# Kernel optimization log

Hardware: AMD Instinct MI355X
Metric: run time of the kernel (lower is better)

Reference implementation:

```python
import jax, jax.numpy as jnp
import numpy as np

H_DIM_EXP = 25  # n = 2**25 = 33,554,432

def setup_inputs() -> dict:
    key = jax.random.key(0)
    x = jax.random.normal(key, (2 ** H_DIM_EXP,), dtype=jnp.float32)
    return {"x": x, "h_dim_exp": H_DIM_EXP}

def reference(x, h_dim_exp):
    # Fast Walsh-Hadamard transform. The original views x as [1,2,2,...,2,1]
    # and applies a (+,-) butterfly along each of the log2(n) axes-of-size-2.
    # Butterfly stages on distinct bits commute, so we process bits from low
    # to high with rank-3 reshapes instead of a rank-(exp+2) tensor.
    y = x
    for i in range(h_dim_exp):
        y = y.reshape(-1, 2, 2 ** i)        # (n/2^{i+1}, 2, 2^i)
        a, b = y[:, 0, :], y[:, 1, :]
        y = jnp.stack([a + b, a - b], axis=1)
    return y.reshape(x.shape)
```

## Files before the change

### kernel.cpp

```cpp
#include <hip/hip_runtime.h>


typedef float vf4 __attribute__((ext_vector_type(4)));

__device__ __forceinline__ float4 ntload(const float4* p) {
  vf4 r = __builtin_nontemporal_load(reinterpret_cast<const vf4*>(p));
  return *reinterpret_cast<float4*>(&r);
}
__device__ __forceinline__ void ntstore(float4* p, float4 v) {
  __builtin_nontemporal_store(*reinterpret_cast<vf4*>(&v),
                              reinterpret_cast<vf4*>(p));
}

__device__ __forceinline__ void bfly(float4& a, float4& b) {
  float ax = a.x, ay = a.y, az = a.z, aw = a.w;
  a.x = ax + b.x; a.y = ay + b.y; a.z = az + b.z; a.w = aw + b.w;
  b.x = ax - b.x; b.y = ay - b.y; b.z = az - b.z; b.w = aw - b.w;
}

__device__ __forceinline__ void cross4(float4 (&v)[16]) {
#pragma unroll
  for (int m = 0; m < 4; ++m) {
#pragma unroll
    for (int k = 0; k < 16; ++k) {
      if (!(k & (1 << m))) bfly(v[k], v[k | (1 << m)]);
    }
  }
}

__global__ __launch_bounds__(256) void wht_pass1(const float4* __restrict__ in4,
                                                 float4* __restrict__ out4) {
  __shared__ float4 lds[4096];
  const int t = threadIdx.x;
  const int base4 = (int)blockIdx.x << 12;
  float4 v[16];
#pragma unroll
  for (int k = 0; k < 16; ++k)
    v[k] = ntload(&in4[base4 + t + (k << 8)]);
#pragma unroll
  for (int k = 0; k < 16; ++k) {
    float4 a = v[k];
    float s0 = a.x + a.y, d0 = a.x - a.y, s1 = a.z + a.w, d1 = a.z - a.w;
    v[k].x = s0 + s1; v[k].y = d0 + d1; v[k].z = s0 - s1; v[k].w = d0 - d1;
  }
  cross4(v);

#pragma unroll
  for (int k = 0; k < 16; ++k) { int q = t + (k << 8); lds[q ^ ((q >> 4) & 15)] = v[k]; }
  __syncthreads();
#pragma unroll
  for (int u = 0; u < 16; ++u) { int q = u + (t << 4); v[u] = lds[q ^ ((q >> 4) & 15)]; }
  cross4(v);

#pragma unroll
  for (int u = 0; u < 16; ++u) { int q = u + (t << 4); lds[q ^ ((q >> 4) & 15)] = v[u]; }
  __syncthreads();
  const int c0 = t & 15, c1 = t >> 4;
#pragma unroll
  for (int u = 0; u < 16; ++u) {
    int q = c0 + (u << 4) + (c1 << 8);
    v[u] = lds[q ^ ((q >> 4) & 15)];
  }
  cross4(v);

#pragma unroll
  for (int u = 0; u < 16; ++u) out4[base4 + c0 + (u << 4) + (c1 << 8)] = v[u];
}

__global__ __launch_bounds__(512) void wht_pass2(float4* __restrict__ b4) {
  __shared__ float4 lds[8192];
  const int t = threadIdx.x;
  const int cb4 = (int)blockIdx.x << 3;
  const int c4 = t & 7;
  const int rlo = t >> 3;
  float4 v[32];
#pragma unroll
  for (int k = 0; k < 32; ++k)
    v[k] = ntload(&b4[((rlo + (k << 6)) << 12) + cb4 + c4]);

#pragma unroll
  for (int m = 0; m < 5; ++m) {
#pragma unroll
    for (int k = 0; k < 32; ++k)
      if (!(k & (1 << m))) bfly(v[k], v[k | (1 << m)]);
  }

  const int rhi6 = t >> 3;

#pragma unroll
  for (int b = 0; b < 2; ++b) {
    if (b) __syncthreads();
#pragma unroll
    for (int k16 = 0; k16 < 16; ++k16)
      lds[((rlo + (k16 << 6)) << 3) + c4] = v[(b << 4) | k16];
    __syncthreads();
#pragma unroll
    for (int j16 = 0; j16 < 16; ++j16)
      v[(b << 4) | j16] = lds[((j16 + (rhi6 << 4)) << 3) + c4];
  }
  cross4(*reinterpret_cast<float4(*)[16]>(&v[0]));
  cross4(*reinterpret_cast<float4(*)[16]>(&v[16]));

#pragma unroll
  for (int b = 0; b < 2; ++b) {
    if (b) __syncthreads();
#pragma unroll
    for (int j16 = 0; j16 < 16; ++j16)
      lds[((j16 + (rhi6 << 4)) << 3) + c4] = v[(b << 4) | j16];
    __syncthreads();
#pragma unroll
    for (int i = 0; i < 16; ++i) {
      int rowkey = ((i >> 2) & 3) | (((t >> 3) & 3) << 2) | ((i & 3) << 4) |
                   ((t >> 5) << 6);
      v[(b << 4) | i] = lds[(rowkey << 3) + c4];
    }
  }
#pragma unroll
  for (int m = 0; m < 2; ++m) {
#pragma unroll
    for (int i = 0; i < 32; ++i)
      if (!(i & (1 << m))) bfly(v[i], v[i | (1 << m)]);
  }

#pragma unroll
  for (int i2 = 0; i2 < 32; ++i2) {
    int b = i2 >> 4, i = i2 & 15;
    int rowkey = ((i >> 2) & 3) | (((t >> 3) & 3) << 2) | ((i & 3) << 4) |
                 ((t >> 5) << 6);
    int row = rowkey | (b << 10);
    ntstore(&b4[(row << 12) + cb4 + c4], v[i2]);
  }
}

extern "C" void kernel_launch(void* const* d_in, const int* in_sizes, int n_in,
                              void* d_out, int out_size, void* d_ws, size_t ws_size,
                              hipStream_t stream) {
  (void)in_sizes; (void)n_in; (void)d_ws; (void)ws_size; (void)out_size;
  const float* x = (const float*)d_in[0];
  float* out = (float*)d_out;
  wht_pass1<<<2048, 256, 0, stream>>>((const float4*)x, (float4*)out);
  wht_pass2<<<512, 512, 0, stream>>>((float4*)out);
}
```

Baseline: 295.0 us.

## Restructure pass2 into narrower 256-thread blocks with swizzled 3x3-bit LDS exchanges

Pass2 now uses 256-thread blocks, each covering 4 float4 columns instead of 8, so twice as many blocks are launched and each uses a quarter of the LDS. The earlier scheme (two 16-way exchanges plus a 2-bit finish) is replaced by two rounds of four 8-row transposes through a XOR-swizzled LDS buffer, each followed by 3 butterfly levels. The aim is higher occupancy, fewer LDS bank conflicts and a smaller shared-memory footprint. The cost is more barriers, and each global row segment shrinks to 64 bytes, which may hurt memory coalescing.

```diff
diff --git a/kernel.cpp b/kernel.cpp
--- a/kernel.cpp
+++ b/kernel.cpp
@@ -67,16 +67,16 @@
   for (int u = 0; u < 16; ++u) out4[base4 + c0 + (u << 4) + (c1 << 8)] = v[u];
 }
 
-__global__ __launch_bounds__(512) void wht_pass2(float4* __restrict__ b4) {
-  __shared__ float4 lds[8192];
+__global__ __launch_bounds__(256, 4) void wht_pass2(float4* __restrict__ b4) {
+  __shared__ float4 lds[2048];
   const int t = threadIdx.x;
-  const int cb4 = (int)blockIdx.x << 3;
-  const int c4 = t & 7;
-  const int rlo = t >> 3;
+  const int cb4 = (int)blockIdx.x << 2;
+  const int c4 = t & 3;
+  const int rA = t >> 2;
   float4 v[32];
 #pragma unroll
   for (int k = 0; k < 32; ++k)
-    v[k] = ntload(&b4[((rlo + (k << 6)) << 12) + cb4 + c4]);
+    v[k] = ntload(&b4[((rA + (k << 6)) << 12) + cb4 + c4]);
 
 #pragma unroll
   for (int m = 0; m < 5; ++m) {
@@ -85,50 +85,59 @@
       if (!(k & (1 << m))) bfly(v[k], v[k | (1 << m)]);
   }
 
-  const int rhi6 = t >> 3;
-
 #pragma unroll
-  for (int b = 0; b < 2; ++b) {
-    if (b) __syncthreads();
+  for (int q = 0; q < 4; ++q) {
+    const int RQ = ((q & 1) << 3) | ((q >> 1) << 4);
+    if (q) __syncthreads();
 #pragma unroll
-    for (int k16 = 0; k16 < 16; ++k16)
-      lds[((rlo + (k16 << 6)) << 3) + c4] = v[(b << 4) | k16];
+    for (int m = 0; m < 8; ++m) {
+      int s = ((rA + (m << 6)) << 2) | c4;
+      lds[s ^ ((s >> 5) & 7)] = v[RQ | m];
+    }
     __syncthreads();
 #pragma unroll
-    for (int j16 = 0; j16 < 16; ++j16)
-      v[(b << 4) | j16] = lds[((j16 + (rhi6 << 4)) << 3) + c4];
-  }
-  cross4(*reinterpret_cast<float4(*)[16]>(&v[0]));
-  cross4(*reinterpret_cast<float4(*)[16]>(&v[16]));
-
-#pragma unroll
-  for (int b = 0; b < 2; ++b) {
-    if (b) __syncthreads();
-#pragma unroll
-    for (int j16 = 0; j16 < 16; ++j16)
-      lds[((j16 + (rhi6 << 4)) << 3) + c4] = v[(b << 4) | j16];
-    __syncthreads();
-#pragma unroll
-    for (int i = 0; i < 16; ++i) {
-      int rowkey = ((i >> 2) & 3) | (((t >> 3) & 3) << 2) | ((i & 3) << 4) |
-                   ((t >> 5) << 6);
-      v[(b << 4) | i] = lds[(rowkey << 3) + c4];
+    for (int jm = 0; jm < 8; ++jm) {
+      int s = ((jm + (rA << 3)) << 2) | c4;
+      v[RQ | jm] = lds[s ^ ((s >> 5) & 7)];
     }
   }
 #pragma unroll
-  for (int m = 0; m < 2; ++m) {
+  for (int m = 0; m < 3; ++m) {
 #pragma unroll
-    for (int i = 0; i < 32; ++i)
-      if (!(i & (1 << m))) bfly(v[i], v[i | (1 << m)]);
+    for (int k = 0; k < 32; ++k)
+      if (!(k & (1 << m))) bfly(v[k], v[k | (1 << m)]);
+  }
+
+  const int rlowC = (t >> 2) & 7;
+  const int rmidC = t >> 5;
+#pragma unroll
+  for (int q = 0; q < 4; ++q) {
+    const int RQ = ((q & 1) << 3) | ((q >> 1) << 4);
+    __syncthreads();
+#pragma unroll
+    for (int jm = 0; jm < 8; ++jm) {
+      int s = ((jm + (rA << 3)) << 2) | c4;
+      lds[s ^ ((s >> 5) & 7)] = v[RQ | jm];
+    }
+    __syncthreads();
+#pragma unroll
+    for (int im = 0; im < 8; ++im) {
+      int s = ((rlowC + (im << 3) + (rmidC << 6)) << 2) | c4;
+      v[RQ | im] = lds[s ^ ((s >> 5) & 7)];
+    }
+  }
+#pragma unroll
+  for (int m = 0; m < 3; ++m) {
+#pragma unroll
+    for (int k = 0; k < 32; ++k)
+      if (!(k & (1 << m))) bfly(v[k], v[k | (1 << m)]);
   }
 
 #pragma unroll
-  for (int i2 = 0; i2 < 32; ++i2) {
-    int b = i2 >> 4, i = i2 & 15;
-    int rowkey = ((i >> 2) & 3) | (((t >> 3) & 3) << 2) | ((i & 3) << 4) |
-                 ((t >> 5) << 6);
-    int row = rowkey | (b << 10);
-    ntstore(&b4[(row << 12) + cb4 + c4], v[i2]);
+  for (int i = 0; i < 32; ++i) {
+    int row = rlowC + ((i & 7) << 3) + (rmidC << 6) + (((i >> 3) & 1) << 9) +
+              ((i >> 4) << 10);
+    ntstore(&b4[(row << 12) + cb4 + c4], v[i]);
   }
 }
 
@@ -139,5 +148,5 @@
   const float* x = (const float*)d_in[0];
   float* out = (float*)d_out;
   wht_pass1<<<2048, 256, 0, stream>>>((const float4*)x, (float4*)out);
-  wht_pass2<<<512, 512, 0, stream>>>((float4*)out);
+  wht_pass2<<<1024, 256, 0, stream>>>((float4*)out);
 }
```

Result: slower. 492.2 us (+66.8%).
